# Optimization experiments

Hardware: AMD Instinct MI355X
Metric: run time of the kernel (lower is better)

## Reference

```python
import jax, jax.numpy as jnp
import numpy as np
from jax import lax

T, IN, H, OUT = 4096, 1024, 2048, 512


def setup_inputs() -> dict:
    key = jax.random.key(0)
    ks = jax.random.split(key, 11)
    s = 1.0 / np.sqrt(IN + H)
    s2 = 1.0 / np.sqrt(2 * H)
    def lin(k, o, i, sc):
        kw, kb = jax.random.split(k)
        W = jax.random.uniform(kw, (o, i), minval=-sc, maxval=sc, dtype=jnp.float32)
        b = jax.random.uniform(kb, (o,), minval=-sc, maxval=sc, dtype=jnp.float32)
        return W, b
    Wi, bi = lin(ks[0], H, IN + H, s)
    Wf, bf = lin(ks[1], H, IN + H, s)
    Wo, bo = lin(ks[2], H, IN + H, s)
    Wc, bc = lin(ks[3], H, IN + H, s)
    W2, b2 = lin(ks[4], OUT, 2 * H, s2)
    x = jax.random.normal(ks[5], (T, IN), dtype=jnp.float32)
    return {"input": x, "Wi": Wi, "bi": bi, "Wf": Wf, "bf": bf,
            "Wo": Wo, "bo": bo, "Wc": Wc, "bc": bc, "W2": W2, "b2": b2}


def reference(input, Wi, bi, Wf, bf, Wo, bo, Wc, bc, W2, b2):
    n_in = input.shape[1]
    # split each gate weight into input part and hidden part (cat(x, h) layout)
    def split(W):
        return W[:, :n_in], W[:, n_in:]
    Wix, Wih = split(Wi); Wfx, Wfh = split(Wf)
    Wox, Woh = split(Wo); Wcx, Wch = split(Wc)
    # precompute the input contribution for all timesteps in one GEMM each
    xi = input @ Wix.T + bi  # [T, H]
    xf = input @ Wfx.T + bf
    xo = input @ Wox.T + bo
    xc = input @ Wcx.T + bc

    def step(carry, xs):
        h, c = carry
        xi_t, xf_t, xo_t, xc_t = xs
        i = jax.nn.sigmoid(xi_t + Wih @ h)
        f = jax.nn.sigmoid(xf_t + Wfh @ h)
        o = jax.nn.sigmoid(xo_t + Woh @ h)
        c_tilde = jnp.tanh(xc_t + Wch @ h)
        c = f * c + i * c_tilde
        h = o * jnp.tanh(c)
        return (h, c), None

    h0 = jnp.zeros((Wih.shape[0],), dtype=input.dtype)
    c0 = jnp.zeros_like(h0)
    (h, c), _ = lax.scan(step, (h0, c0), (xi, xf, xo, xc))
    output = W2 @ jnp.concatenate([h, c]) + b2
    return output, h
```

## Files before the change

### kernel.cpp

```cpp
#include <hip/hip_runtime.h>
#include <stdint.h>

#define T_STEPS 4096
#define IN_DIM  1024
#define H_DIM   2048
#define OUT_DIM 512
#define W_STRIDE 3072
#define NBLK    256
#define NTHR    512
#define POLL_GUARD 65536

typedef __attribute__((ext_vector_type(4))) float floatx4;

__device__ __forceinline__ int swz(int q) { return q ^ ((q >> 3) & 7); }

__device__ __forceinline__ float fsigmoid(float v) {
  return __builtin_amdgcn_rcpf(1.f + __expf(-v));
}
__device__ __forceinline__ float ftanh(float v) {
  return 1.f - 2.f * __builtin_amdgcn_rcpf(1.f + __expf(2.f * v));
}
__device__ __forceinline__ unsigned umin2(unsigned a, unsigned b) {
  return a < b ? a : b;
}

#define FMA4(acc, wq, v) do {                                                 \
    acc = fmaf(wq.x, v.x, acc); acc = fmaf(wq.y, v.y, acc);                   \
    acc = fmaf(wq.z, v.z, acc); acc = fmaf(wq.w, v.w, acc); } while (0)
#define WDECL(r) floatx4 wx##r##_0, wx##r##_1,                                \
    wh##r##_0, wh##r##_1, wh##r##_2, wh##r##_3
#define WLOAD(r) do {                                                         \
    const float* rx_ = wxb + (size_t)(r) * W_STRIDE;                          \
    const float* rh_ = whb + (size_t)(r) * W_STRIDE;                          \
    wx##r##_0 = *(const floatx4*)(rx_ + 0);                                   \
    wx##r##_1 = *(const floatx4*)(rx_ + 4);                                   \
    wh##r##_0 = *(const floatx4*)(rh_ + 0);                                   \
    wh##r##_1 = *(const floatx4*)(rh_ + 4);                                   \
    wh##r##_2 = *(const floatx4*)(rh_ + 8);                                   \
    wh##r##_3 = *(const floatx4*)(rh_ + 12); } while (0)
#define WPIN(r) asm volatile("" : "+v"(wx##r##_0), "+v"(wx##r##_1),           \
    "+v"(wh##r##_0), "+v"(wh##r##_1), "+v"(wh##r##_2), "+v"(wh##r##_3))
#define XFMA(r) do { FMA4(ac##r, wx##r##_0, xa);                              \
    FMA4(ac##r, wx##r##_1, xb); } while (0)
#define HFMAK(k) do {                                                         \
    const floatx4 v = *(const floatx4*)(hl + a_h##k);                         \
    FMA4(ac0, wh0_##k, v); FMA4(ac1, wh1_##k, v);                             \
    FMA4(ac2, wh2_##k, v); FMA4(ac3, wh3_##k, v);                             \
    FMA4(ac4, wh4_##k, v); FMA4(ac5, wh5_##k, v);                             \
    FMA4(ac6, wh6_##k, v); FMA4(ac7, wh7_##k, v); } while (0)
#define WRED(acc, r) do { float a_ = acc;                                     \
    a_ += __shfl_down(a_, 32, 64); a_ += __shfl_down(a_, 16, 64);             \
    a_ += __shfl_down(a_, 8, 64);  a_ += __shfl_down(a_, 4, 64);              \
    a_ += __shfl_down(a_, 2, 64);  a_ += __shfl_down(a_, 1, 64);              \
    if (lane == 0) red[wv * 8 + (r)] = a_; } while (0)

__global__ __launch_bounds__(NTHR, 2)
void lstm_scan(const float* __restrict__ Wi, const float* __restrict__ Wf,
               const float* __restrict__ Wo, const float* __restrict__ Wc,
               const float* __restrict__ bi, const float* __restrict__ bff,
               const float* __restrict__ bo, const float* __restrict__ bc,
               const float* __restrict__ x,
               unsigned long long* __restrict__ hcomm,
               float* __restrict__ hbuf,
               float* __restrict__ cbuf)
{
  __shared__ float hl[512 * 4];
  __shared__ float red[8 * 8];
  __shared__ float bl[32];
  __shared__ float cl[8];

  const int tid  = threadIdx.x;
  const int b    = blockIdx.x;
  const int row0 = b << 3;
  const int grp  = tid >> 7;
  const int u    = tid & 127;
  const int wv   = tid >> 6;
  const int lane = tid & 63;

  const float* Wsel = (grp == 0) ? Wi : (grp == 1) ? Wf : (grp == 2) ? Wo : Wc;
  const float* wxb = Wsel + (size_t)row0 * W_STRIDE + (u << 3);
  const float* whb = Wsel + (size_t)row0 * W_STRIDE + IN_DIM + (u << 4);

  WDECL(0); WDECL(1); WDECL(2); WDECL(3);
  WDECL(4); WDECL(5); WDECL(6); WDECL(7);
  WLOAD(0); WLOAD(1); WLOAD(2); WLOAD(3);
  WLOAD(4); WLOAD(5); WLOAD(6); WLOAD(7);
  WPIN(0); WPIN(1); WPIN(2); WPIN(3);
  WPIN(4); WPIN(5); WPIN(6); WPIN(7);

  if (tid < 32) {
    const float* Bsel = (tid < 8) ? bi : (tid < 16) ? bff : (tid < 24) ? bo : bc;
    bl[tid] = Bsel[row0 + (tid & 7)];
  }
  if (tid < 8) cl[tid] = 0.f;
  __syncthreads();

  const int a_h0 = swz(4 * u + 0) << 2;
  const int a_h1 = swz(4 * u + 1) << 2;
  const int a_h2 = swz(4 * u + 2) << 2;
  const int a_h3 = swz(4 * u + 3) << 2;
  const int hv0 = (swz((tid >> 2) +   0) << 2) + (tid & 3);
  const int hv1 = (swz((tid >> 2) + 128) << 2) + (tid & 3);
  const int hv2 = (swz((tid >> 2) + 256) << 2) + (tid & 3);
  const int hv3 = (swz((tid >> 2) + 384) << 2) + (tid & 3);

  float hlast = 0.f;
  int   alive = 1;

  for (int t = 0; t < T_STEPS; ++t) {
    const float* xp = x + ((size_t)t << 10) + (u << 3);
    const floatx4 xa = *(const floatx4*)(xp);
    const floatx4 xb = *(const floatx4*)(xp + 4);

    unsigned long long* hb = hcomm + ((size_t)(t & 1) << 11);
    const unsigned tt = (unsigned)t;
    unsigned long long p0, p1, p2, p3;
    p0 = __hip_atomic_load(&hb[tid], __ATOMIC_RELAXED,
                           __HIP_MEMORY_SCOPE_AGENT);
    p1 = __hip_atomic_load(&hb[tid + 512], __ATOMIC_RELAXED,
                           __HIP_MEMORY_SCOPE_AGENT);
    p2 = __hip_atomic_load(&hb[tid + 1024], __ATOMIC_RELAXED,
                           __HIP_MEMORY_SCOPE_AGENT);
    p3 = __hip_atomic_load(&hb[tid + 1536], __ATOMIC_RELAXED,
                           __HIP_MEMORY_SCOPE_AGENT);

    float ac0 = 0.f, ac1 = 0.f, ac2 = 0.f, ac3 = 0.f,
          ac4 = 0.f, ac5 = 0.f, ac6 = 0.f, ac7 = 0.f;
    XFMA(0); XFMA(1); XFMA(2); XFMA(3);
    XFMA(4); XFMA(5); XFMA(6); XFMA(7);

    {
      unsigned mn = umin2(umin2((unsigned)(p0 >> 32), (unsigned)(p1 >> 32)),
                          umin2((unsigned)(p2 >> 32), (unsigned)(p3 >> 32)));
      int guard = 0;
      while (alive && mn < tt) {
        if (++guard > POLL_GUARD) { alive = 0; break; }
        __builtin_amdgcn_s_sleep(1);
        p0 = __hip_atomic_load(&hb[tid], __ATOMIC_RELAXED,
                               __HIP_MEMORY_SCOPE_AGENT);
        p1 = __hip_atomic_load(&hb[tid + 512], __ATOMIC_RELAXED,
                               __HIP_MEMORY_SCOPE_AGENT);
        p2 = __hip_atomic_load(&hb[tid + 1024], __ATOMIC_RELAXED,
                               __HIP_MEMORY_SCOPE_AGENT);
        p3 = __hip_atomic_load(&hb[tid + 1536], __ATOMIC_RELAXED,
                               __HIP_MEMORY_SCOPE_AGENT);
        mn = umin2(umin2((unsigned)(p0 >> 32), (unsigned)(p1 >> 32)),
                   umin2((unsigned)(p2 >> 32), (unsigned)(p3 >> 32)));
      }
    }
    hl[hv0] = __uint_as_float((unsigned)p0);
    hl[hv1] = __uint_as_float((unsigned)p1);
    hl[hv2] = __uint_as_float((unsigned)p2);
    hl[hv3] = __uint_as_float((unsigned)p3);
    __syncthreads();

    HFMAK(0); HFMAK(1); HFMAK(2); HFMAK(3);

    WRED(ac0, 0); WRED(ac1, 1); WRED(ac2, 2); WRED(ac3, 3);
    WRED(ac4, 4); WRED(ac5, 5); WRED(ac6, 6); WRED(ac7, 7);
    __syncthreads();

    if (tid < 8) {
      const int rr = tid;
      const float pi = bl[rr]      + red[0 * 8 + rr] + red[1 * 8 + rr];
      const float pf = bl[8 + rr]  + red[2 * 8 + rr] + red[3 * 8 + rr];
      const float po = bl[16 + rr] + red[4 * 8 + rr] + red[5 * 8 + rr];
      const float pc = bl[24 + rr] + red[6 * 8 + rr] + red[7 * 8 + rr];
      const float iv = fsigmoid(pi);
      const float fv = fsigmoid(pf);
      const float ov = fsigmoid(po);
      const float ct = ftanh(pc);
      const float cn = fv * cl[rr] + iv * ct;
      cl[rr] = cn;
      const float hv = ov * ftanh(cn);
      hlast = hv;
      const unsigned long long pk =
          ((unsigned long long)(unsigned)(t + 1) << 32) |
          (unsigned long long)__float_as_uint(hv);
      __hip_atomic_store(&hcomm[(((size_t)((t + 1) & 1)) << 11) + row0 + rr],
                         pk, __ATOMIC_RELAXED, __HIP_MEMORY_SCOPE_AGENT);
    }
  }

  if (tid < 8) {
    hbuf[row0 + tid] = hlast;
    cbuf[row0 + tid] = cl[tid];
  }
}

__global__ __launch_bounds__(256)
void final_kernel(const float* __restrict__ W2, const float* __restrict__ b2,
                  const float* __restrict__ hfin, const float* __restrict__ cfin,
                  float* __restrict__ out)
{
  const int wv   = threadIdx.x >> 6;
  const int lane = threadIdx.x & 63;
  const int row  = (blockIdx.x << 2) + wv;
  const float* wr = W2 + (size_t)row * (2 * H_DIM);
  float acc = 0.f;
#pragma unroll 4
  for (int k = lane; k < H_DIM; k += 64) {
    acc = fmaf(wr[k], hfin[k], acc);
    acc = fmaf(wr[H_DIM + k], cfin[k], acc);
  }
#pragma unroll
  for (int off = 32; off > 0; off >>= 1) acc += __shfl_down(acc, off, 64);
  if (lane == 0) out[row] = acc + b2[row];
}

__global__ __launch_bounds__(256)
void copy_h_kernel(const float* __restrict__ hfin, float* __restrict__ out)
{
  const int i = blockIdx.x * 256 + threadIdx.x;
  if (i < H_DIM) out[OUT_DIM + i] = hfin[i];
}

extern "C" void kernel_launch(void* const* d_in, const int* in_sizes, int n_in,
                              void* d_out, int out_size, void* d_ws, size_t ws_size,
                              hipStream_t stream)
{
  const float* x   = (const float*)d_in[0];
  const float* Wi  = (const float*)d_in[1];
  const float* bi  = (const float*)d_in[2];
  const float* Wf  = (const float*)d_in[3];
  const float* bff = (const float*)d_in[4];
  const float* Wo  = (const float*)d_in[5];
  const float* bo  = (const float*)d_in[6];
  const float* Wc  = (const float*)d_in[7];
  const float* bc  = (const float*)d_in[8];
  const float* W2  = (const float*)d_in[9];
  const float* b2  = (const float*)d_in[10];
  float* out = (float*)d_out;

  char* ws = (char*)d_ws;
  unsigned long long* hcomm = (unsigned long long*)ws;
  float* hbuf = (float*)(ws + 2 * H_DIM * sizeof(unsigned long long));
  float* cbuf = hbuf + H_DIM;

  hipMemsetAsync(hcomm, 0, 2 * H_DIM * sizeof(unsigned long long), stream);

  lstm_scan<<<dim3(NBLK), dim3(NTHR), 0, stream>>>(
      Wi, Wf, Wo, Wc, bi, bff, bo, bc, x, hcomm, hbuf, cbuf);
  final_kernel<<<dim3(OUT_DIM / 4), 256, 0, stream>>>(W2, b2, hbuf, cbuf, out);
  copy_h_kernel<<<dim3((H_DIM + 255) / 256), 256, 0, stream>>>(hbuf, out);
}
```

Measured before the change: 16.62 ms.

## Map one wavefront per hidden row covering all four gates, double-buffer h

Reassigns work so each 64-lane wavefront owns one hidden row and holds all four gates' weight slices for that row in registers, instead of splitting gates across 128-thread groups. The per-step cross-wave reduction through shared memory, and the second __syncthreads it needed, are removed; each wave's lane 0 finishes its own gate math and publishes h. The h shared buffer is double-buffered with a plain strided layout instead of the swizzle, so one barrier per step is enough. The interleaved 256-element stride may change LDS and global access efficiency, and register pressure stays similar.

```diff
diff --git a/kernel.cpp b/kernel.cpp
--- a/kernel.cpp
+++ b/kernel.cpp
@@ -12,8 +12,6 @@
 
 typedef __attribute__((ext_vector_type(4))) float floatx4;
 
-__device__ __forceinline__ int swz(int q) { return q ^ ((q >> 3) & 7); }
-
 __device__ __forceinline__ float fsigmoid(float v) {
   return __builtin_amdgcn_rcpf(1.f + __expf(-v));
 }
@@ -27,32 +25,34 @@
 #define FMA4(acc, wq, v) do {                                                 \
     acc = fmaf(wq.x, v.x, acc); acc = fmaf(wq.y, v.y, acc);                   \
     acc = fmaf(wq.z, v.z, acc); acc = fmaf(wq.w, v.w, acc); } while (0)
-#define WDECL(r) floatx4 wx##r##_0, wx##r##_1,                                \
-    wh##r##_0, wh##r##_1, wh##r##_2, wh##r##_3
-#define WLOAD(r) do {                                                         \
-    const float* rx_ = wxb + (size_t)(r) * W_STRIDE;                          \
-    const float* rh_ = whb + (size_t)(r) * W_STRIDE;                          \
-    wx##r##_0 = *(const floatx4*)(rx_ + 0);                                   \
-    wx##r##_1 = *(const floatx4*)(rx_ + 4);                                   \
-    wh##r##_0 = *(const floatx4*)(rh_ + 0);                                   \
-    wh##r##_1 = *(const floatx4*)(rh_ + 4);                                   \
-    wh##r##_2 = *(const floatx4*)(rh_ + 8);                                   \
-    wh##r##_3 = *(const floatx4*)(rh_ + 12); } while (0)
-#define WPIN(r) asm volatile("" : "+v"(wx##r##_0), "+v"(wx##r##_1),           \
-    "+v"(wh##r##_0), "+v"(wh##r##_1), "+v"(wh##r##_2), "+v"(wh##r##_3))
-#define XFMA(r) do { FMA4(ac##r, wx##r##_0, xa);                              \
-    FMA4(ac##r, wx##r##_1, xb); } while (0)
-#define HFMAK(k) do {                                                         \
-    const floatx4 v = *(const floatx4*)(hl + a_h##k);                         \
-    FMA4(ac0, wh0_##k, v); FMA4(ac1, wh1_##k, v);                             \
-    FMA4(ac2, wh2_##k, v); FMA4(ac3, wh3_##k, v);                             \
-    FMA4(ac4, wh4_##k, v); FMA4(ac5, wh5_##k, v);                             \
-    FMA4(ac6, wh6_##k, v); FMA4(ac7, wh7_##k, v); } while (0)
-#define WRED(acc, r) do { float a_ = acc;                                     \
-    a_ += __shfl_down(a_, 32, 64); a_ += __shfl_down(a_, 16, 64);             \
-    a_ += __shfl_down(a_, 8, 64);  a_ += __shfl_down(a_, 4, 64);              \
-    a_ += __shfl_down(a_, 2, 64);  a_ += __shfl_down(a_, 1, 64);              \
-    if (lane == 0) red[wv * 8 + (r)] = a_; } while (0)
+#define GDECL(g) floatx4 wx##g##_0, wx##g##_1, wx##g##_2, wx##g##_3,          \
+    wh##g##_0, wh##g##_1, wh##g##_2, wh##g##_3,                               \
+    wh##g##_4, wh##g##_5, wh##g##_6, wh##g##_7
+#define GLOAD(g, P) do {                                                      \
+    wx##g##_0 = *(const floatx4*)((P) +    0);                                \
+    wx##g##_1 = *(const floatx4*)((P) +  256);                                \
+    wx##g##_2 = *(const floatx4*)((P) +  512);                                \
+    wx##g##_3 = *(const floatx4*)((P) +  768);                                \
+    wh##g##_0 = *(const floatx4*)((P) + 1024);                                \
+    wh##g##_1 = *(const floatx4*)((P) + 1280);                                \
+    wh##g##_2 = *(const floatx4*)((P) + 1536);                                \
+    wh##g##_3 = *(const floatx4*)((P) + 1792);                                \
+    wh##g##_4 = *(const floatx4*)((P) + 2048);                                \
+    wh##g##_5 = *(const floatx4*)((P) + 2304);                                \
+    wh##g##_6 = *(const floatx4*)((P) + 2560);                                \
+    wh##g##_7 = *(const floatx4*)((P) + 2816); } while (0)
+#define GPIN(g) asm volatile("" : "+v"(wx##g##_0), "+v"(wx##g##_1),           \
+    "+v"(wx##g##_2), "+v"(wx##g##_3), "+v"(wh##g##_0), "+v"(wh##g##_1),       \
+    "+v"(wh##g##_2), "+v"(wh##g##_3), "+v"(wh##g##_4), "+v"(wh##g##_5),       \
+    "+v"(wh##g##_6), "+v"(wh##g##_7))
+#define HFMA(i) do {                                                          \
+    const floatx4 v = *(const floatx4*)(hr + (i) * 256);                      \
+    FMA4(a0, wh0_##i, v); FMA4(a1, wh1_##i, v);                               \
+    FMA4(a2, wh2_##i, v); FMA4(a3, wh3_##i, v); } while (0)
+#define RED(a) do {                                                           \
+    a += __shfl_down(a, 32, 64); a += __shfl_down(a, 16, 64);                 \
+    a += __shfl_down(a, 8, 64);  a += __shfl_down(a, 4, 64);                  \
+    a += __shfl_down(a, 2, 64);  a += __shfl_down(a, 1, 64); } while (0)
 
 __global__ __launch_bounds__(NTHR, 2)
 void lstm_scan(const float* __restrict__ Wi, const float* __restrict__ Wf,
@@ -64,53 +64,29 @@
                float* __restrict__ hbuf,
                float* __restrict__ cbuf)
 {
-  __shared__ float hl[512 * 4];
-  __shared__ float red[8 * 8];
-  __shared__ float bl[32];
-  __shared__ float cl[8];
-
-  const int tid  = threadIdx.x;
-  const int b    = blockIdx.x;
-  const int row0 = b << 3;
-  const int grp  = tid >> 7;
-  const int u    = tid & 127;
-  const int wv   = tid >> 6;
-  const int lane = tid & 63;
-
-  const float* Wsel = (grp == 0) ? Wi : (grp == 1) ? Wf : (grp == 2) ? Wo : Wc;
-  const float* wxb = Wsel + (size_t)row0 * W_STRIDE + (u << 3);
-  const float* whb = Wsel + (size_t)row0 * W_STRIDE + IN_DIM + (u << 4);
-
-  WDECL(0); WDECL(1); WDECL(2); WDECL(3);
-  WDECL(4); WDECL(5); WDECL(6); WDECL(7);
-  WLOAD(0); WLOAD(1); WLOAD(2); WLOAD(3);
-  WLOAD(4); WLOAD(5); WLOAD(6); WLOAD(7);
-  WPIN(0); WPIN(1); WPIN(2); WPIN(3);
-  WPIN(4); WPIN(5); WPIN(6); WPIN(7);
-
-  if (tid < 32) {
-    const float* Bsel = (tid < 8) ? bi : (tid < 16) ? bff : (tid < 24) ? bo : bc;
-    bl[tid] = Bsel[row0 + (tid & 7)];
-  }
-  if (tid < 8) cl[tid] = 0.f;
-  __syncthreads();
-
-  const int a_h0 = swz(4 * u + 0) << 2;
-  const int a_h1 = swz(4 * u + 1) << 2;
-  const int a_h2 = swz(4 * u + 2) << 2;
-  const int a_h3 = swz(4 * u + 3) << 2;
-  const int hv0 = (swz((tid >> 2) +   0) << 2) + (tid & 3);
-  const int hv1 = (swz((tid >> 2) + 128) << 2) + (tid & 3);
-  const int hv2 = (swz((tid >> 2) + 256) << 2) + (tid & 3);
-  const int hv3 = (swz((tid >> 2) + 384) << 2) + (tid & 3);
-
-  float hlast = 0.f;
+  __shared__ float hl[2][H_DIM];
+
+  const int tid = threadIdx.x;
+  const int b   = blockIdx.x;
+  const int w   = tid >> 6;
+  const int l   = tid & 63;
+  const int row = (b << 3) + w;
+
+  const size_t wb = (size_t)row * W_STRIDE + ((size_t)l << 2);
+  GDECL(0); GDECL(1); GDECL(2); GDECL(3);
+  GLOAD(0, Wi + wb); GLOAD(1, Wf + wb); GLOAD(2, Wo + wb); GLOAD(3, Wc + wb);
+  GPIN(0); GPIN(1); GPIN(2); GPIN(3);
+
+  const float bia = bi[row], bfa = bff[row], boa = bo[row], bca = bc[row];
+  float creg = 0.f, hlast = 0.f;
   int   alive = 1;
 
   for (int t = 0; t < T_STEPS; ++t) {
-    const float* xp = x + ((size_t)t << 10) + (u << 3);
-    const floatx4 xa = *(const floatx4*)(xp);
-    const floatx4 xb = *(const floatx4*)(xp + 4);
+    const float* xp = x + ((size_t)t << 10) + (l << 2);
+    const floatx4 x0 = *(const floatx4*)(xp);
+    const floatx4 x1 = *(const floatx4*)(xp + 256);
+    const floatx4 x2 = *(const floatx4*)(xp + 512);
+    const floatx4 x3 = *(const floatx4*)(xp + 768);
 
     unsigned long long* hb = hcomm + ((size_t)(t & 1) << 11);
     const unsigned tt = (unsigned)t;
@@ -124,10 +100,11 @@
     p3 = __hip_atomic_load(&hb[tid + 1536], __ATOMIC_RELAXED,
                            __HIP_MEMORY_SCOPE_AGENT);
 
-    float ac0 = 0.f, ac1 = 0.f, ac2 = 0.f, ac3 = 0.f,
-          ac4 = 0.f, ac5 = 0.f, ac6 = 0.f, ac7 = 0.f;
-    XFMA(0); XFMA(1); XFMA(2); XFMA(3);
-    XFMA(4); XFMA(5); XFMA(6); XFMA(7);
+    float a0 = 0.f, a1 = 0.f, a2 = 0.f, a3 = 0.f;
+    FMA4(a0, wx0_0, x0); FMA4(a0, wx0_1, x1); FMA4(a0, wx0_2, x2); FMA4(a0, wx0_3, x3);
+    FMA4(a1, wx1_0, x0); FMA4(a1, wx1_1, x1); FMA4(a1, wx1_2, x2); FMA4(a1, wx1_3, x3);
+    FMA4(a2, wx2_0, x0); FMA4(a2, wx2_1, x1); FMA4(a2, wx2_2, x2); FMA4(a2, wx2_3, x3);
+    FMA4(a3, wx3_0, x0); FMA4(a3, wx3_1, x1); FMA4(a3, wx3_2, x2); FMA4(a3, wx3_3, x3);
 
     {
       unsigned mn = umin2(umin2((unsigned)(p0 >> 32), (unsigned)(p1 >> 32)),
@@ -148,43 +125,48 @@
                    umin2((unsigned)(p2 >> 32), (unsigned)(p3 >> 32)));
       }
     }
-    hl[hv0] = __uint_as_float((unsigned)p0);
-    hl[hv1] = __uint_as_float((unsigned)p1);
-    hl[hv2] = __uint_as_float((unsigned)p2);
-    hl[hv3] = __uint_as_float((unsigned)p3);
+
+    {
+      float* hs = hl[t & 1];
+      hs[tid]        = __uint_as_float((unsigned)p0);
+      hs[tid + 512]  = __uint_as_float((unsigned)p1);
+      hs[tid + 1024] = __uint_as_float((unsigned)p2);
+      hs[tid + 1536] = __uint_as_float((unsigned)p3);
+    }
     __syncthreads();
 
-    HFMAK(0); HFMAK(1); HFMAK(2); HFMAK(3);
-
-    WRED(ac0, 0); WRED(ac1, 1); WRED(ac2, 2); WRED(ac3, 3);
-    WRED(ac4, 4); WRED(ac5, 5); WRED(ac6, 6); WRED(ac7, 7);
-    __syncthreads();
-
-    if (tid < 8) {
-      const int rr = tid;
-      const float pi = bl[rr]      + red[0 * 8 + rr] + red[1 * 8 + rr];
-      const float pf = bl[8 + rr]  + red[2 * 8 + rr] + red[3 * 8 + rr];
-      const float po = bl[16 + rr] + red[4 * 8 + rr] + red[5 * 8 + rr];
-      const float pc = bl[24 + rr] + red[6 * 8 + rr] + red[7 * 8 + rr];
+    {
+      const float* hr = hl[t & 1] + (l << 2);
+      HFMA(0); HFMA(1); HFMA(2); HFMA(3);
+      HFMA(4); HFMA(5); HFMA(6); HFMA(7);
+    }
+
+    RED(a0); RED(a1); RED(a2); RED(a3);
+
+    if (l == 0) {
+      const float pi = bia + a0;
+      const float pf = bfa + a1;
+      const float po = boa + a2;
+      const float pc = bca + a3;
       const float iv = fsigmoid(pi);
       const float fv = fsigmoid(pf);
       const float ov = fsigmoid(po);
       const float ct = ftanh(pc);
-      const float cn = fv * cl[rr] + iv * ct;
-      cl[rr] = cn;
+      const float cn = fv * creg + iv * ct;
+      creg = cn;
       const float hv = ov * ftanh(cn);
       hlast = hv;
       const unsigned long long pk =
           ((unsigned long long)(unsigned)(t + 1) << 32) |
           (unsigned long long)__float_as_uint(hv);
-      __hip_atomic_store(&hcomm[(((size_t)((t + 1) & 1)) << 11) + row0 + rr],
+      __hip_atomic_store(&hcomm[(((size_t)((t + 1) & 1)) << 11) + row],
                          pk, __ATOMIC_RELAXED, __HIP_MEMORY_SCOPE_AGENT);
     }
   }
 
-  if (tid < 8) {
-    hbuf[row0 + tid] = hlast;
-    cbuf[row0 + tid] = cl[tid];
+  if (l == 0) {
+    hbuf[row] = hlast;
+    cbuf[row] = creg;
   }
 }
 
```

Measured after the change: 21.68 ms. +30.5%, slower.
